# Kernel optimization log

Measured on AMD Instinct MI355X. Metric: run time of the kernel, lower is better.

The kernel has to match this reference:

```python
import jax, jax.numpy as jnp
import numpy as np
from math import sqrt

B, L, S = 4, 2048, 2048
D_MODEL, H = 1024, 16
E = D_MODEL // H  # head dim = 64


def setup_inputs() -> dict:
    key = jax.random.key(0)
    ks = jax.random.split(key, 11)
    s = 1.0 / sqrt(D_MODEL)
    return {
        "queries": jax.random.normal(ks[0], (B, L, D_MODEL), jnp.float32),
        "keys": jax.random.normal(ks[1], (B, S, D_MODEL), jnp.float32),
        "values": jax.random.normal(ks[2], (B, S, D_MODEL), jnp.float32),
        "Wq": jax.random.normal(ks[3], (D_MODEL, D_MODEL), jnp.float32) * s,
        "bq": jax.random.normal(ks[4], (D_MODEL,), jnp.float32) * s,
        "Wk": jax.random.normal(ks[5], (D_MODEL, D_MODEL), jnp.float32) * s,
        "bk": jax.random.normal(ks[6], (D_MODEL,), jnp.float32) * s,
        "Wv": jax.random.normal(ks[7], (D_MODEL, D_MODEL), jnp.float32) * s,
        "bv": jax.random.normal(ks[8], (D_MODEL,), jnp.float32) * s,
        "Wo": jax.random.normal(ks[9], (D_MODEL, D_MODEL), jnp.float32) * s,
        "bo": jax.random.normal(ks[10], (D_MODEL,), jnp.float32) * s,
    }


def reference(queries, keys, values, Wq, bq, Wk, bk, Wv, bv, Wo, bo):
    # QKV projections, split heads: [B, L/S, H, E]
    q = (queries @ Wq + bq).reshape(B, L, H, E)
    k = (keys @ Wk + bk).reshape(B, S, H, E)
    v = (values @ Wv + bv).reshape(B, S, H, E)
    scale = 1.0 / sqrt(E)
    scores = jnp.einsum('blhe,bshe->bhls', q, k)  # [B,H,L,S]
    A = jax.nn.softmax(scale * scores, axis=-1)   # dropout is identity in eval
    out = jnp.einsum('bhls,bshd->blhd', A, v).reshape(B, L, H * E)
    return out @ Wo + bo
```

## Files before the change

kernel.cpp:

```cpp
#include <hip/hip_runtime.h>
#include <hip/hip_bf16.h>

typedef unsigned short u16;
typedef unsigned int u32;
using short8 = __attribute__((ext_vector_type(8))) short;
using f32x4  = __attribute__((ext_vector_type(4))) float;
using f32x16 = __attribute__((ext_vector_type(16))) float;
using u32x2  = __attribute__((ext_vector_type(2))) unsigned int;
using u32x4  = __attribute__((ext_vector_type(4))) unsigned int;

#define B_  4
#define L_  2048
#define S_  2048
#define DM  1024
#define H_  16
#define E_  64

__device__ __forceinline__ u16 f2bf(float f) {
  union { float f; unsigned u; } v; v.f = f;
  unsigned u = v.u;
  unsigned r = (u + 0x7fffu + ((u >> 16) & 1u)) >> 16;
  return (u16)r;
}

__device__ __forceinline__ float exp2a(float x) {
  float r; asm("v_exp_f32 %0, %1" : "=v"(r) : "v"(x)); return r;
}

__device__ __forceinline__ u32 cvtpk(float lo, float hi) {
  u32 r; asm("v_cvt_pk_bf16_f32 %0, %1, %2" : "=v"(r) : "v"(lo), "v"(hi));
  return r;
}

__device__ __forceinline__ f32x4 mfma16(short8 a, short8 b, f32x4 c) {
  return __builtin_amdgcn_mfma_f32_16x16x32_bf16(a, b, c, 0, 0, 0);
}

__device__ __forceinline__ f32x16 mfma32(short8 a, short8 b, f32x16 c) {
  return __builtin_amdgcn_mfma_f32_32x32x16_bf16(a, b, c, 0, 0, 0);
}

__device__ __forceinline__ void gload_lds16(const u16* g, u16* l) {
  __builtin_amdgcn_global_load_lds(
      (const __attribute__((address_space(1))) unsigned int*)(const void*)g,
      (__attribute__((address_space(3))) unsigned int*)(void*)l, 16, 0, 0);
}

__global__ __launch_bounds__(256) void cvt_all(const float* __restrict__ s0,
                                               const float* __restrict__ s1,
                                               const float* __restrict__ s2,
                                               u16* __restrict__ d0,
                                               u16* __restrict__ d1,
                                               u16* __restrict__ d2) {
  const float* s = blockIdx.y == 0 ? s0 : blockIdx.y == 1 ? s1 : s2;
  u16* d = blockIdx.y == 0 ? d0 : blockIdx.y == 1 ? d1 : d2;
  int i = (blockIdx.x * 256 + threadIdx.x) * 4;
  f32x4 v = *(const f32x4*)(s + i);
  u32x2 o;
  o.x = cvtpk(v.x, v.y);
  o.y = cvtpk(v.z, v.w);
  *(u32x2*)(d + i) = o;
}

__global__ __launch_bounds__(256) void transp_all(const float* __restrict__ w0,
                                                  const float* __restrict__ w1,
                                                  const float* __restrict__ w2,
                                                  const float* __restrict__ w3,
                                                  u16* __restrict__ t0,
                                                  u16* __restrict__ t1,
                                                  u16* __restrict__ t2,
                                                  u16* __restrict__ t3) {
  const float* W = blockIdx.z == 0 ? w0 : blockIdx.z == 1 ? w1 :
                   blockIdx.z == 2 ? w2 : w3;
  u16* Wt = blockIdx.z == 0 ? t0 : blockIdx.z == 1 ? t1 :
            blockIdx.z == 2 ? t2 : t3;
  __shared__ float t[32][33];
  int tx = threadIdx.x & 31, ty = (threadIdx.x >> 5) & 7;
#pragma unroll
  for (int j = 0; j < 32; j += 8)
    t[ty + j][tx] = W[(size_t)(blockIdx.y * 32 + ty + j) * DM + blockIdx.x * 32 + tx];
  __syncthreads();
#pragma unroll
  for (int j = 0; j < 32; j += 8)
    Wt[(size_t)(blockIdx.x * 32 + ty + j) * DM + blockIdx.y * 32 + tx] = f2bf(t[tx][ty + j]);
}

template <int EPI>
__device__ __forceinline__ void gemm_body(const u16* __restrict__ A,
                                          const u16* __restrict__ Bt,
                                          const float* __restrict__ bias,
                                          void* __restrict__ Cout,
                                          int M, int N, int K, float oscale,
                                          int bx, int by) {
  __shared__ u16 lA[128 * 32];
  __shared__ u16 lB[128 * 32];
  const int tid = threadIdx.x, wid = tid >> 6, lane = tid & 63;
  const int lr = lane & 15, lh = lane >> 4;
  const int m0 = by * 128, n0 = bx * 128;
  const int wr = wid >> 1, wc = wid & 1;

  f32x4 acc[4][4];
#pragma unroll
  for (int m = 0; m < 4; m++)
#pragma unroll
    for (int n = 0; n < 4; n++) acc[m][n] = (f32x4){0.f, 0.f, 0.f, 0.f};

  const int srow = wid * 16 + (lane >> 2);
  const int scol = (lane & 3) * 8;

  for (int k0 = 0; k0 < K; k0 += 32) {
#pragma unroll
    for (int p = 0; p < 2; p++) {
      int r = p * 64 + srow;
      gload_lds16(A + (size_t)(m0 + r) * K + k0 + scol, lA + (p * 64 + wid * 16) * 32);
      gload_lds16(Bt + (size_t)(n0 + r) * K + k0 + scol, lB + (p * 64 + wid * 16) * 32);
    }
    __syncthreads();
    short8 af[4], bf[4];
#pragma unroll
    for (int m = 0; m < 4; m++)
      af[m] = *(const short8*)(lA + (wr * 64 + m * 16 + lr) * 32 + lh * 8);
#pragma unroll
    for (int n = 0; n < 4; n++)
      bf[n] = *(const short8*)(lB + (wc * 64 + n * 16 + lr) * 32 + lh * 8);
#pragma unroll
    for (int m = 0; m < 4; m++)
#pragma unroll
      for (int n = 0; n < 4; n++) acc[m][n] = mfma16(af[m], bf[n], acc[m][n]);
    __syncthreads();
  }

#pragma unroll
  for (int m = 0; m < 4; m++) {
    int grow0 = m0 + wr * 64 + m * 16 + lh * 4;
#pragma unroll
    for (int n = 0; n < 4; n++) {
      int gcol = n0 + wc * 64 + n * 16 + lr;
      float bi = bias[gcol];
      float v0 = (acc[m][n][0] + bi) * oscale;
      float v1 = (acc[m][n][1] + bi) * oscale;
      float v2 = (acc[m][n][2] + bi) * oscale;
      float v3 = (acc[m][n][3] + bi) * oscale;
      if constexpr (EPI == 2) {
        float* C = (float*)Cout;
        C[(size_t)(grow0 + 0) * N + gcol] = v0;
        C[(size_t)(grow0 + 1) * N + gcol] = v1;
        C[(size_t)(grow0 + 2) * N + gcol] = v2;
        C[(size_t)(grow0 + 3) * N + gcol] = v3;
      } else {
        u32 p01 = cvtpk(v0, v1), p23 = cvtpk(v2, v3);
        u16* C = (u16*)Cout;
#pragma unroll
        for (int r = 0; r < 4; r++) {
          u32 pk = r < 2 ? p01 : p23;
          u16 bv = (r & 1) ? (u16)(pk >> 16) : (u16)(pk & 0xffff);
          int grow = grow0 + r;
          if constexpr (EPI == 0) {
            C[(size_t)grow * N + gcol] = bv;
          } else {
            int bb = grow >> 11, sl = grow & 2047;
            C[((size_t)(bb * DM) + gcol) * S_ + sl] = bv;
          }
        }
      }
    }
  }
}

__global__ __launch_bounds__(256) void gemm_qkv(
    const u16* __restrict__ qb, const u16* __restrict__ kb, const u16* __restrict__ vb,
    const u16* __restrict__ WqT, const u16* __restrict__ WkT, const u16* __restrict__ WvT,
    const float* __restrict__ bq, const float* __restrict__ bk, const float* __restrict__ bv,
    u16* __restrict__ Qp, u16* __restrict__ Kp, u16* __restrict__ Vt, float qsc) {
  const int z = blockIdx.z;
  if (z == 0)
    gemm_body<0>(qb, WqT, bq, Qp, B_ * L_, DM, DM, qsc, blockIdx.x, blockIdx.y);
  else if (z == 1)
    gemm_body<0>(kb, WkT, bk, Kp, B_ * L_, DM, DM, 1.0f, blockIdx.x, blockIdx.y);
  else
    gemm_body<1>(vb, WvT, bv, Vt, B_ * L_, DM, DM, 1.0f, blockIdx.x, blockIdx.y);
}

__global__ __launch_bounds__(256) void gemm_out(const u16* __restrict__ A,
                                                const u16* __restrict__ Bt,
                                                const float* __restrict__ bias,
                                                float* __restrict__ C) {
  gemm_body<2>(A, Bt, bias, C, B_ * L_, DM, DM, 1.0f, blockIdx.x, blockIdx.y);
}

__global__ __launch_bounds__(256, 3) void attn(const u16* __restrict__ Q,
                                               const u16* __restrict__ Kp,
                                               const u16* __restrict__ Vt,
                                               u16* __restrict__ O) {
  __shared__ u16 lK[2][64 * 64];
  __shared__ u16 lV[2][64 * 64];
  const int tid = threadIdx.x, wid = tid >> 6, lane = tid & 63;
  const int l31 = lane & 31, hi = lane >> 5;

  int lin = blockIdx.x + gridDim.x * (blockIdx.y + gridDim.y * blockIdx.z);
  int swz = (lin & 7) * 128 + (lin >> 3);
  const int b = swz >> 8, h = (swz >> 4) & 15, q0 = (swz & 15) * 128;
  const int qrow = q0 + wid * 32 + l31;

  const u16* Qb = Q + ((size_t)(b * L_ + qrow)) * DM + h * E_ + hi * 8;
  short8 qf[4];
#pragma unroll
  for (int s = 0; s < 4; s++) qf[s] = *(const short8*)(Qb + s * 16);

  f32x16 o[2];
#pragma unroll
  for (int et = 0; et < 2; et++)
#pragma unroll
    for (int r = 0; r < 16; r++) o[et][r] = 0.f;
  float m_r = -3.0e38f, l_r = 0.f;

  const u16* Kb = Kp + ((size_t)(b * S_)) * DM + h * E_;
  const u16* Vb = Vt + ((size_t)(b * DM + h * E_)) * S_;
  const int g_r = lane >> 3;
  const int g_c = ((lane & 7) ^ g_r) * 8;
  const int sxk = (l31 & 7) * 8;
  const int hi4 = hi * 4, hi8 = hi * 8;

  auto stage = [&](int buf, int kb) {
#pragma unroll
    for (int p = 0; p < 2; p++) {
      int row = p * 32 + wid * 8 + g_r;
      gload_lds16(Kb + (size_t)(kb + row) * DM + g_c, lK[buf] + (p * 32 + wid * 8) * 64);
      gload_lds16(Vb + (size_t)row * S_ + kb + g_c, lV[buf] + (p * 32 + wid * 8) * 64);
    }
  };

  stage(0, 0);
  const int NT = S_ / 64;
  for (int it = 0; it < NT; ++it) {
    const int buf = it & 1;
    __syncthreads();
    if (it + 1 < NT) stage(buf ^ 1, (it + 1) * 64);

    f32x16 sc[2];
    __builtin_amdgcn_s_setprio(1);
#pragma unroll
    for (int kt = 0; kt < 2; kt++) {
      f32x16 a;
#pragma unroll
      for (int r = 0; r < 16; r++) a[r] = 0.f;
      const u16* kp = lK[buf] + (kt * 32 + l31) * 64;
#pragma unroll
      for (int s = 0; s < 4; s++) {
        short8 kf = *(const short8*)(kp + ((s * 16 + hi8) ^ sxk));
        a = mfma32(kf, qf[s], a);
      }
      sc[kt] = a;
    }
    __builtin_amdgcn_s_setprio(0);

    float tm = sc[0][0];
#pragma unroll
    for (int r = 1; r < 16; r++) tm = fmaxf(tm, sc[0][r]);
#pragma unroll
    for (int r = 0; r < 16; r++) tm = fmaxf(tm, sc[1][r]);
    tm = fmaxf(tm, __shfl_xor(tm, 32));

    if (__any(tm > m_r + 8.f)) {
      float mn = fmaxf(m_r, tm);
      float al = exp2a(m_r - mn);
      m_r = mn;
      l_r *= al;
#pragma unroll
      for (int et = 0; et < 2; et++)
#pragma unroll
        for (int r = 0; r < 16; r++) o[et][r] *= al;
    }

    u32 wp[2][8];
    float rs = 0.f;
#pragma unroll
    for (int kt = 0; kt < 2; kt++)
#pragma unroll
      for (int i = 0; i < 8; i++) {
        float p0 = exp2a(sc[kt][2 * i] - m_r);
        float p1 = exp2a(sc[kt][2 * i + 1] - m_r);
        rs += p0 + p1;
        wp[kt][i] = cvtpk(p0, p1);
      }
    rs += __shfl_xor(rs, 32);
    l_r += rs;

    __builtin_amdgcn_s_setprio(1);
#pragma unroll
    for (int et = 0; et < 2; et++) {
      const u16* vp = lV[buf] + (et * 32 + l31) * 64;
#pragma unroll
      for (int kt = 0; kt < 2; kt++)
#pragma unroll
        for (int su = 0; su < 2; su++) {
          int koff = kt * 32 + su * 16 + hi4;
          u32x2 lo = *(const u32x2*)(vp + (koff ^ sxk));
          u32x2 hp = *(const u32x2*)(vp + ((koff + 8) ^ sxk));
          u32x4 vv = {lo.x, lo.y, hp.x, hp.y};
          u32x4 pv = {wp[kt][su * 4 + 0], wp[kt][su * 4 + 1],
                      wp[kt][su * 4 + 2], wp[kt][su * 4 + 3]};
          o[et] = mfma32(*(const short8*)&vv, *(const short8*)&pv, o[et]);
        }
    }
    __builtin_amdgcn_s_setprio(0);
  }

  float inv = 1.f / l_r;
  u16* Ob = O + ((size_t)(b * L_ + qrow)) * DM + h * E_;
#pragma unroll
  for (int et = 0; et < 2; et++)
#pragma unroll
    for (int t = 0; t < 4; t++) {
      u32x2 pk;
      pk.x = cvtpk(o[et][4 * t] * inv, o[et][4 * t + 1] * inv);
      pk.y = cvtpk(o[et][4 * t + 2] * inv, o[et][4 * t + 3] * inv);
      *(u32x2*)(Ob + et * 32 + t * 8 + hi4) = pk;
    }
}

extern "C" void kernel_launch(void* const* d_in, const int* in_sizes, int n_in,
                              void* d_out, int out_size, void* d_ws, size_t ws_size,
                              hipStream_t stream) {
  (void)in_sizes; (void)n_in; (void)out_size; (void)ws_size;
  const float* q  = (const float*)d_in[0];
  const float* k  = (const float*)d_in[1];
  const float* v  = (const float*)d_in[2];
  const float* Wq = (const float*)d_in[3];
  const float* bq = (const float*)d_in[4];
  const float* Wk = (const float*)d_in[5];
  const float* bk = (const float*)d_in[6];
  const float* Wv = (const float*)d_in[7];
  const float* bv = (const float*)d_in[8];
  const float* Wo = (const float*)d_in[9];
  const float* bo = (const float*)d_in[10];

  char* w = (char*)d_ws;
  const size_t ACT = (size_t)B_ * L_ * DM * 2;
  const size_t WT  = (size_t)DM * DM * 2;
  u16* qb  = (u16*)w; w += ACT;
  u16* kb  = (u16*)w; w += ACT;
  u16* vb  = (u16*)w; w += ACT;
  u16* WqT = (u16*)w; w += WT;
  u16* WkT = (u16*)w; w += WT;
  u16* WvT = (u16*)w; w += WT;
  u16* WoT = (u16*)w; w += WT;
  u16* Qp  = (u16*)w; w += ACT;
  u16* Kp  = (u16*)w; w += ACT;
  u16* Vt  = (u16*)w; w += ACT;
  u16* At  = (u16*)w; w += ACT;

  const int M = B_ * L_;
  cvt_all<<<dim3(M * DM / (4 * 256), 3), 256, 0, stream>>>(q, k, v, qb, kb, vb);
  transp_all<<<dim3(32, 32, 4), 256, 0, stream>>>(Wq, Wk, Wv, Wo, WqT, WkT, WvT, WoT);

  const float QSC = 0.125f * 1.44269504089f;
  gemm_qkv<<<dim3(DM / 128, M / 128, 3), 256, 0, stream>>>(
      qb, kb, vb, WqT, WkT, WvT, bq, bk, bv, Qp, Kp, Vt, QSC);

  attn<<<dim3(L_ / 128, H_, B_), 256, 0, stream>>>(Qp, Kp, Vt, At);

  gemm_out<<<dim3(DM / 128, M / 128), 256, 0, stream>>>(At, WoT, bo, (float*)d_out);
}
```

Measured before the change: 242.2 us.

## Double-buffer GEMM LDS tiles and widen attention KV tiles with MFMA row sums

The projection GEMM now double-buffers its LDS A/B tiles and prefetches the next K-slice before computing, which removes one barrier per iteration. The attention kernel processes 128 keys per tile instead of 64, with wider swizzled LDS layouts, and uses a tree-reduced row max. The softmax row sum is now computed by an extra MFMA against a ones vector instead of VALU adds and a shuffle. This doubles LDS use in both kernels and drops the attention occupancy hint, so fewer blocks may fit per CU.

Measured after the change: 305.3 us. 1.26x slower.

```diff
diff --git a/kernel.cpp b/kernel.cpp
--- a/kernel.cpp
+++ b/kernel.cpp
@@ -92,8 +92,8 @@
                                           void* __restrict__ Cout,
                                           int M, int N, int K, float oscale,
                                           int bx, int by) {
-  __shared__ u16 lA[128 * 32];
-  __shared__ u16 lB[128 * 32];
+  __shared__ u16 lA[2][128 * 32];
+  __shared__ u16 lB[2][128 * 32];
   const int tid = threadIdx.x, wid = tid >> 6, lane = tid & 63;
   const int lr = lane & 15, lh = lane >> 4;
   const int m0 = by * 128, n0 = bx * 128;
@@ -108,26 +108,33 @@
   const int srow = wid * 16 + (lane >> 2);
   const int scol = (lane & 3) * 8;
 
-  for (int k0 = 0; k0 < K; k0 += 32) {
+  auto stage = [&](int buf, int k0) {
 #pragma unroll
     for (int p = 0; p < 2; p++) {
       int r = p * 64 + srow;
-      gload_lds16(A + (size_t)(m0 + r) * K + k0 + scol, lA + (p * 64 + wid * 16) * 32);
-      gload_lds16(Bt + (size_t)(n0 + r) * K + k0 + scol, lB + (p * 64 + wid * 16) * 32);
-    }
+      gload_lds16(A + (size_t)(m0 + r) * K + k0 + scol, lA[buf] + (p * 64 + wid * 16) * 32);
+      gload_lds16(Bt + (size_t)(n0 + r) * K + k0 + scol, lB[buf] + (p * 64 + wid * 16) * 32);
+    }
+  };
+
+  const int NS = K / 32;
+  stage(0, 0);
+#pragma unroll 2
+  for (int ks = 0; ks < NS; ks++) {
+    const int buf = ks & 1;
     __syncthreads();
+    if (ks + 1 < NS) stage(buf ^ 1, (ks + 1) * 32);
     short8 af[4], bf[4];
 #pragma unroll
     for (int m = 0; m < 4; m++)
-      af[m] = *(const short8*)(lA + (wr * 64 + m * 16 + lr) * 32 + lh * 8);
+      af[m] = *(const short8*)(lA[buf] + (wr * 64 + m * 16 + lr) * 32 + lh * 8);
 #pragma unroll
     for (int n = 0; n < 4; n++)
-      bf[n] = *(const short8*)(lB + (wc * 64 + n * 16 + lr) * 32 + lh * 8);
+      bf[n] = *(const short8*)(lB[buf] + (wc * 64 + n * 16 + lr) * 32 + lh * 8);
 #pragma unroll
     for (int m = 0; m < 4; m++)
 #pragma unroll
       for (int n = 0; n < 4; n++) acc[m][n] = mfma16(af[m], bf[n], acc[m][n]);
-    __syncthreads();
   }
 
 #pragma unroll
@@ -188,12 +195,12 @@
   gemm_body<2>(A, Bt, bias, C, B_ * L_, DM, DM, 1.0f, blockIdx.x, blockIdx.y);
 }
 
-__global__ __launch_bounds__(256, 3) void attn(const u16* __restrict__ Q,
-                                               const u16* __restrict__ Kp,
-                                               const u16* __restrict__ Vt,
-                                               u16* __restrict__ O) {
-  __shared__ u16 lK[2][64 * 64];
-  __shared__ u16 lV[2][64 * 64];
+__global__ __launch_bounds__(256) void attn(const u16* __restrict__ Q,
+                                            const u16* __restrict__ Kp,
+                                            const u16* __restrict__ Vt,
+                                            u16* __restrict__ O) {
+  __shared__ u16 lK[2][128 * 64];
+  __shared__ u16 lV[2][64 * 128];
   const int tid = threadIdx.x, wid = tid >> 6, lane = tid & 63;
   const int l31 = lane & 31, hi = lane >> 5;
 
@@ -207,116 +214,131 @@
 #pragma unroll
   for (int s = 0; s < 4; s++) qf[s] = *(const short8*)(Qb + s * 16);
 
-  f32x16 o[2];
-#pragma unroll
-  for (int et = 0; et < 2; et++)
-#pragma unroll
-    for (int r = 0; r < 16; r++) o[et][r] = 0.f;
-  float m_r = -3.0e38f, l_r = 0.f;
+  short8 ones;
+#pragma unroll
+  for (int i = 0; i < 8; i++) ones[i] = (short)0x3F80;
+
+  f32x16 o0, o1, lac;
+#pragma unroll
+  for (int r = 0; r < 16; r++) { o0[r] = 0.f; o1[r] = 0.f; lac[r] = 0.f; }
+  float m_r = -3.0e38f;
 
   const u16* Kb = Kp + ((size_t)(b * S_)) * DM + h * E_;
   const u16* Vb = Vt + ((size_t)(b * DM + h * E_)) * S_;
-  const int g_r = lane >> 3;
-  const int g_c = ((lane & 7) ^ g_r) * 8;
+
+  const int krow = wid * 8 + (lane >> 3);
+  const u16* srcK = Kb + (size_t)krow * DM + (((lane & 7) ^ (krow & 7)) * 8);
+  const int vrow = wid * 4 + (lane >> 4);
+  const u16* srcV = Vb + (size_t)vrow * S_ + (((lane & 15) ^ (vrow & 15)) * 8);
+
   const int sxk = (l31 & 7) * 8;
+  const int sxv = (l31 & 15) * 8;
   const int hi4 = hi * 4, hi8 = hi * 8;
 
-  auto stage = [&](int buf, int kb) {
-#pragma unroll
-    for (int p = 0; p < 2; p++) {
-      int row = p * 32 + wid * 8 + g_r;
-      gload_lds16(Kb + (size_t)(kb + row) * DM + g_c, lK[buf] + (p * 32 + wid * 8) * 64);
-      gload_lds16(Vb + (size_t)row * S_ + kb + g_c, lV[buf] + (p * 32 + wid * 8) * 64);
-    }
+  auto stage = [&](int buf, int t) {
+    const u16* sk = srcK + (size_t)t * 128 * DM;
+    const u16* sv = srcV + (size_t)t * 128;
+#pragma unroll
+    for (int p = 0; p < 4; p++)
+      gload_lds16(sk + (size_t)p * 32 * DM, lK[buf] + p * 2048 + wid * 512);
+#pragma unroll
+    for (int p = 0; p < 4; p++)
+      gload_lds16(sv + (size_t)p * 16 * S_, lV[buf] + p * 2048 + wid * 512);
   };
 
   stage(0, 0);
-  const int NT = S_ / 64;
+  const int NT = S_ / 128;
+#pragma unroll 2
   for (int it = 0; it < NT; ++it) {
     const int buf = it & 1;
     __syncthreads();
-    if (it + 1 < NT) stage(buf ^ 1, (it + 1) * 64);
-
-    f32x16 sc[2];
+    if (it + 1 < NT) stage(buf ^ 1, it + 1);
+
+    f32x16 sc[4];
+    const u16* kbase = lK[buf] + l31 * 64;
     __builtin_amdgcn_s_setprio(1);
 #pragma unroll
-    for (int kt = 0; kt < 2; kt++) {
+    for (int kt = 0; kt < 4; kt++) {
       f32x16 a;
 #pragma unroll
       for (int r = 0; r < 16; r++) a[r] = 0.f;
-      const u16* kp = lK[buf] + (kt * 32 + l31) * 64;
 #pragma unroll
       for (int s = 0; s < 4; s++) {
-        short8 kf = *(const short8*)(kp + ((s * 16 + hi8) ^ sxk));
+        short8 kf = *(const short8*)(kbase + kt * 2048 + ((s * 16 + hi8) ^ sxk));
         a = mfma32(kf, qf[s], a);
       }
       sc[kt] = a;
     }
     __builtin_amdgcn_s_setprio(0);
 
-    float tm = sc[0][0];
-#pragma unroll
-    for (int r = 1; r < 16; r++) tm = fmaxf(tm, sc[0][r]);
-#pragma unroll
-    for (int r = 0; r < 16; r++) tm = fmaxf(tm, sc[1][r]);
+    f32x16 mA, mB;
+#pragma unroll
+    for (int r = 0; r < 16; r++) mA[r] = fmaxf(sc[0][r], sc[1][r]);
+#pragma unroll
+    for (int r = 0; r < 16; r++) mB[r] = fmaxf(sc[2][r], sc[3][r]);
+#pragma unroll
+    for (int r = 0; r < 16; r++) mA[r] = fmaxf(mA[r], mB[r]);
+#pragma unroll
+    for (int r = 0; r < 8; r++) mA[r] = fmaxf(mA[r], mA[r + 8]);
+#pragma unroll
+    for (int r = 0; r < 4; r++) mA[r] = fmaxf(mA[r], mA[r + 4]);
+    float tm = fmaxf(fmaxf(mA[0], mA[1]), fmaxf(mA[2], mA[3]));
     tm = fmaxf(tm, __shfl_xor(tm, 32));
 
     if (__any(tm > m_r + 8.f)) {
       float mn = fmaxf(m_r, tm);
       float al = exp2a(m_r - mn);
       m_r = mn;
-      l_r *= al;
-#pragma unroll
-      for (int et = 0; et < 2; et++)
-#pragma unroll
-        for (int r = 0; r < 16; r++) o[et][r] *= al;
-    }
-
-    u32 wp[2][8];
-    float rs = 0.f;
-#pragma unroll
-    for (int kt = 0; kt < 2; kt++)
-#pragma unroll
-      for (int i = 0; i < 8; i++) {
-        float p0 = exp2a(sc[kt][2 * i] - m_r);
-        float p1 = exp2a(sc[kt][2 * i + 1] - m_r);
-        rs += p0 + p1;
-        wp[kt][i] = cvtpk(p0, p1);
+      lac[0] *= al;
+#pragma unroll
+      for (int r = 0; r < 16; r++) { o0[r] *= al; o1[r] *= al; }
+    }
+
+    u32 wp[4][8];
+#pragma unroll
+    for (int kt = 0; kt < 4; kt++) {
+      f32x16 d = sc[kt] - m_r;
+#pragma unroll
+      for (int i = 0; i < 8; i++)
+        wp[kt][i] = cvtpk(exp2a(d[2 * i]), exp2a(d[2 * i + 1]));
+    }
+
+    const u16* vbase = lV[buf] + l31 * 128;
+    __builtin_amdgcn_s_setprio(1);
+#pragma unroll
+    for (int kt = 0; kt < 4; kt++)
+#pragma unroll
+      for (int su = 0; su < 2; su++) {
+        u32x4 pw = {wp[kt][su * 4 + 0], wp[kt][su * 4 + 1],
+                    wp[kt][su * 4 + 2], wp[kt][su * 4 + 3]};
+        short8 pf = *(const short8*)&pw;
+        int ka = ((kt * 32 + su * 16 + hi4) ^ sxv);
+        int kb2 = ((kt * 32 + su * 16 + hi4 + 8) ^ sxv);
+        u32x2 lo0 = *(const u32x2*)(vbase + ka);
+        u32x2 hp0 = *(const u32x2*)(vbase + kb2);
+        u32x4 vv0 = {lo0.x, lo0.y, hp0.x, hp0.y};
+        o0 = mfma32(*(const short8*)&vv0, pf, o0);
+        u32x2 lo1 = *(const u32x2*)(vbase + 4096 + ka);
+        u32x2 hp1 = *(const u32x2*)(vbase + 4096 + kb2);
+        u32x4 vv1 = {lo1.x, lo1.y, hp1.x, hp1.y};
+        o1 = mfma32(*(const short8*)&vv1, pf, o1);
+        lac = mfma32(ones, pf, lac);
       }
-    rs += __shfl_xor(rs, 32);
-    l_r += rs;
-
-    __builtin_amdgcn_s_setprio(1);
-#pragma unroll
-    for (int et = 0; et < 2; et++) {
-      const u16* vp = lV[buf] + (et * 32 + l31) * 64;
-#pragma unroll
-      for (int kt = 0; kt < 2; kt++)
-#pragma unroll
-        for (int su = 0; su < 2; su++) {
-          int koff = kt * 32 + su * 16 + hi4;
-          u32x2 lo = *(const u32x2*)(vp + (koff ^ sxk));
-          u32x2 hp = *(const u32x2*)(vp + ((koff + 8) ^ sxk));
-          u32x4 vv = {lo.x, lo.y, hp.x, hp.y};
-          u32x4 pv = {wp[kt][su * 4 + 0], wp[kt][su * 4 + 1],
-                      wp[kt][su * 4 + 2], wp[kt][su * 4 + 3]};
-          o[et] = mfma32(*(const short8*)&vv, *(const short8*)&pv, o[et]);
-        }
-    }
     __builtin_amdgcn_s_setprio(0);
   }
 
-  float inv = 1.f / l_r;
+  float inv = 1.f / lac[0];
   u16* Ob = O + ((size_t)(b * L_ + qrow)) * DM + h * E_;
 #pragma unroll
-  for (int et = 0; et < 2; et++)
-#pragma unroll
-    for (int t = 0; t < 4; t++) {
-      u32x2 pk;
-      pk.x = cvtpk(o[et][4 * t] * inv, o[et][4 * t + 1] * inv);
-      pk.y = cvtpk(o[et][4 * t + 2] * inv, o[et][4 * t + 3] * inv);
-      *(u32x2*)(Ob + et * 32 + t * 8 + hi4) = pk;
-    }
+  for (int t = 0; t < 4; t++) {
+    u32x2 pk;
+    pk.x = cvtpk(o0[4 * t] * inv, o0[4 * t + 1] * inv);
+    pk.y = cvtpk(o0[4 * t + 2] * inv, o0[4 * t + 3] * inv);
+    *(u32x2*)(Ob + t * 8 + hi4) = pk;
+    pk.x = cvtpk(o1[4 * t] * inv, o1[4 * t + 1] * inv);
+    pk.y = cvtpk(o1[4 * t + 2] * inv, o1[4 * t + 3] * inv);
+    *(u32x2*)(Ob + 32 + t * 8 + hi4) = pk;
+  }
 }
 
 extern "C" void kernel_launch(void* const* d_in, const int* in_sizes, int n_in,
```

## Double attention block to 512 threads with 256 query rows per block

Applied to the files above, without the earlier changes.

The attention kernel now runs 8 waves per block covering 256 query rows, so each K/V tile staged into LDS is shared by twice as many queries. That halves the global-to-LDS traffic per query and lets each thread issue a single staging load per tile. The grid becomes a flat 512 blocks with a new swizzle, and the row-max reduction is rewritten as a tree to shorten the dependency chain. The cost is fewer blocks, a dropped occupancy hint, and possible tail or occupancy effects from the larger block.

Result: faster. 232.8 us (-3.9%).

```diff
diff --git a/kernel.cpp b/kernel.cpp
--- a/kernel.cpp
+++ b/kernel.cpp
@@ -188,18 +188,19 @@
   gemm_body<2>(A, Bt, bias, C, B_ * L_, DM, DM, 1.0f, blockIdx.x, blockIdx.y);
 }
 
-__global__ __launch_bounds__(256, 3) void attn(const u16* __restrict__ Q,
-                                               const u16* __restrict__ Kp,
-                                               const u16* __restrict__ Vt,
-                                               u16* __restrict__ O) {
+__global__ __launch_bounds__(512) void attn(const u16* __restrict__ Q,
+                                            const u16* __restrict__ Kp,
+                                            const u16* __restrict__ Vt,
+                                            u16* __restrict__ O) {
   __shared__ u16 lK[2][64 * 64];
   __shared__ u16 lV[2][64 * 64];
   const int tid = threadIdx.x, wid = tid >> 6, lane = tid & 63;
   const int l31 = lane & 31, hi = lane >> 5;
 
-  int lin = blockIdx.x + gridDim.x * (blockIdx.y + gridDim.y * blockIdx.z);
-  int swz = (lin & 7) * 128 + (lin >> 3);
-  const int b = swz >> 8, h = (swz >> 4) & 15, q0 = (swz & 15) * 128;
+  int lin = blockIdx.x;
+  int swz = (lin & 7) * 64 + (lin >> 3);
+  const int bh = swz >> 3, q0 = (swz & 7) * 256;
+  const int b = bh >> 4, h = bh & 15;
   const int qrow = q0 + wid * 32 + l31;
 
   const u16* Qb = Q + ((size_t)(b * L_ + qrow)) * DM + h * E_ + hi * 8;
@@ -216,18 +217,17 @@
 
   const u16* Kb = Kp + ((size_t)(b * S_)) * DM + h * E_;
   const u16* Vb = Vt + ((size_t)(b * DM + h * E_)) * S_;
-  const int g_r = lane >> 3;
-  const int g_c = ((lane & 7) ^ g_r) * 8;
+
+  const int srow = wid * 8 + (lane >> 3);
+  const u16* srcK = Kb + (size_t)srow * DM + ((lane & 7) ^ (srow & 7)) * 8;
+  const u16* srcV = Vb + (size_t)srow * S_ + ((lane & 7) ^ (srow & 7)) * 8;
+
   const int sxk = (l31 & 7) * 8;
   const int hi4 = hi * 4, hi8 = hi * 8;
 
   auto stage = [&](int buf, int kb) {
-#pragma unroll
-    for (int p = 0; p < 2; p++) {
-      int row = p * 32 + wid * 8 + g_r;
-      gload_lds16(Kb + (size_t)(kb + row) * DM + g_c, lK[buf] + (p * 32 + wid * 8) * 64);
-      gload_lds16(Vb + (size_t)row * S_ + kb + g_c, lV[buf] + (p * 32 + wid * 8) * 64);
-    }
+    gload_lds16(srcK + (size_t)kb * DM, lK[buf] + wid * 512);
+    gload_lds16(srcV + kb, lV[buf] + wid * 512);
   };
 
   stage(0, 0);
@@ -238,27 +238,30 @@
     if (it + 1 < NT) stage(buf ^ 1, (it + 1) * 64);
 
     f32x16 sc[2];
+    const u16* kbase = lK[buf] + l31 * 64;
     __builtin_amdgcn_s_setprio(1);
 #pragma unroll
     for (int kt = 0; kt < 2; kt++) {
       f32x16 a;
 #pragma unroll
       for (int r = 0; r < 16; r++) a[r] = 0.f;
-      const u16* kp = lK[buf] + (kt * 32 + l31) * 64;
 #pragma unroll
       for (int s = 0; s < 4; s++) {
-        short8 kf = *(const short8*)(kp + ((s * 16 + hi8) ^ sxk));
+        short8 kf = *(const short8*)(kbase + kt * 2048 + ((s * 16 + hi8) ^ sxk));
         a = mfma32(kf, qf[s], a);
       }
       sc[kt] = a;
     }
     __builtin_amdgcn_s_setprio(0);
 
-    float tm = sc[0][0];
-#pragma unroll
-    for (int r = 1; r < 16; r++) tm = fmaxf(tm, sc[0][r]);
-#pragma unroll
-    for (int r = 0; r < 16; r++) tm = fmaxf(tm, sc[1][r]);
+    f32x16 mA;
+#pragma unroll
+    for (int r = 0; r < 16; r++) mA[r] = fmaxf(sc[0][r], sc[1][r]);
+#pragma unroll
+    for (int r = 0; r < 8; r++) mA[r] = fmaxf(mA[r], mA[r + 8]);
+#pragma unroll
+    for (int r = 0; r < 4; r++) mA[r] = fmaxf(mA[r], mA[r + 4]);
+    float tm = fmaxf(fmaxf(mA[0], mA[1]), fmaxf(mA[2], mA[3]));
     tm = fmaxf(tm, __shfl_xor(tm, 32));
 
     if (__any(tm > m_r + 8.f)) {
@@ -358,7 +361,7 @@
   gemm_qkv<<<dim3(DM / 128, M / 128, 3), 256, 0, stream>>>(
       qb, kb, vb, WqT, WkT, WvT, bq, bk, bv, Qp, Kp, Vt, QSC);
 
-  attn<<<dim3(L_ / 128, H_, B_), 256, 0, stream>>>(Qp, Kp, Vt, At);
+  attn<<<dim3(512), 512, 0, stream>>>(Qp, Kp, Vt, At);
 
   gemm_out<<<dim3(DM / 128, M / 128), 256, 0, stream>>>(At, WoT, bo, (float*)d_out);
 }
```
